# Kernel tuning notes

Hardware: AMD Instinct MI355X
Metric: run time of the kernel (lower is better)

Reference implementation:

```python
import jax, jax.numpy as jnp
import numpy as np

NEG_SLOPE = 0.01  # torch leaky_relu default

def leaky_relu(x):
    return jnp.where(x >= 0, x, NEG_SLOPE * x)

def setup_inputs() -> dict:
    key = jax.random.key(0)
    k1, k2, k3, k4, k5, k6 = jax.random.split(key, 6)
    B, N, D, E = 4, 20000, 128, 100000
    s = 1.0 / np.sqrt(D)
    embeddings = jax.random.normal(k1, (B, N, D), dtype=jnp.float32)
    edges_ij = jax.random.randint(k2, (E, 2), 0, N, dtype=jnp.int64)
    W6 = jax.random.uniform(k3, (D, D), jnp.float32, -s, s)   # theta6 (in,out)
    W7 = jax.random.uniform(k4, (D, D), jnp.float32, -s, s)   # theta7 (in,out)
    w5 = jax.random.uniform(k5, (3 * D,), jnp.float32, -1.0 / np.sqrt(3 * D), 1.0 / np.sqrt(3 * D))  # theta5
    w_noop = jax.random.uniform(k6, (D,), jnp.float32, -s, s)  # noop
    return {"embeddings": embeddings, "edges_ij": edges_ij, "W6": W6, "W7": W7, "w5": w5, "w_noop": w_noop}

def reference(embeddings, edges_ij, W6, W7, w5, w_noop):
    B, N, D = embeddings.shape
    u = edges_ij[:, 0]
    v = edges_ij[:, 1]
    g = embeddings.sum(axis=1)                      # [B,D] (normalize=False)
    g_proj = g @ W6                                  # [B,D]
    node_proj = jnp.einsum('bnd,de->bne', embeddings, W7)  # [B,N,D]
    # theta5(leaky_relu(cat[g,i,j])) == lrelu(g)@w5_g + lrelu(i)@w5_i + lrelu(j)@w5_j
    # (leaky_relu is elementwise, theta5 has no bias), so project per-node THEN
    # gather scalars per edge — avoids the [B,E,3D] concat intermediate.
    w5_g, w5_i, w5_j = w5[:D], w5[D:2 * D], w5[2 * D:]
    qg = leaky_relu(g_proj) @ w5_g                   # [B]
    qi = leaky_relu(node_proj) @ w5_i                # [B,N]
    qj = leaky_relu(node_proj) @ w5_j                # [B,N]
    edge_q = qg[:, None] + qi[:, u] + qj[:, v]       # [B,E]
    noop_q = (g @ w_noop)[:, None]                   # [B,1]
    return jnp.concatenate([edge_q, noop_q], axis=1)  # [B,E+1]
```

## Files before the change

### kernel.cpp

```cpp
#include <hip/hip_runtime.h>
#include <hip/hip_bf16.h>

#define B_ 4
#define N_ 20000
#define D_ 128
#define E_ 100000

typedef __attribute__((ext_vector_type(8))) short bf16x8;
typedef __attribute__((ext_vector_type(4))) float f32x4;


__global__ void k_prep(const float* __restrict__ W7, __hip_bfloat16* __restrict__ w7t,
                       const unsigned* __restrict__ ew, int* __restrict__ flag) {
    if (blockIdx.x == 64) {
        if (threadIdx.x < 64) {
            unsigned v = ew[2 * threadIdx.x + 1];
            unsigned long long any = __ballot(v != 0u);
            if (threadIdx.x == 0) *flag = (any == 0ULL) ? 1 : 0;
        }
        return;
    }
    int idx = blockIdx.x * 256 + threadIdx.x;
    int k = idx >> 7, e = idx & 127;
    w7t[e * 128 + k] = __float2bfloat16(W7[idx]);
}

__global__ __launch_bounds__(256, 2) void k_main(
    const float* __restrict__ emb, const __hip_bfloat16* __restrict__ w7t,
    const float* __restrict__ w5, float* __restrict__ g,
    float* __restrict__ qi, float* __restrict__ qj)
{
    __shared__ __hip_bfloat16 sA[128][136];
    __shared__ __hip_bfloat16 sB[128][136];
    __shared__ float sred[8][128];

    const int t  = threadIdx.x;
    const int b  = blockIdx.y;
    const int n0 = blockIdx.x * 128;

    {
        const int c4 = t & 31;
        const int r0 = t >> 5;
        float gp0 = 0.f, gp1 = 0.f, gp2 = 0.f, gp3 = 0.f;
        #pragma unroll
        for (int i = 0; i < 16; ++i) {
            int r = r0 + 8 * i;
            int n = n0 + r;
            float4 v = make_float4(0.f, 0.f, 0.f, 0.f);
            if (n < N_) v = ((const float4*)(emb + ((size_t)b * N_ + n) * D_))[c4];
            gp0 += v.x; gp1 += v.y; gp2 += v.z; gp3 += v.w;
            union { short4 s4; __hip_bfloat16 h[4]; } pk;
            pk.h[0] = __float2bfloat16(v.x);
            pk.h[1] = __float2bfloat16(v.y);
            pk.h[2] = __float2bfloat16(v.z);
            pk.h[3] = __float2bfloat16(v.w);
            *reinterpret_cast<short4*>(&sA[r][4 * c4]) = pk.s4;
        }
        sred[r0][4 * c4]     = gp0;
        sred[r0][4 * c4 + 1] = gp1;
        sred[r0][4 * c4 + 2] = gp2;
        sred[r0][4 * c4 + 3] = gp3;
    }
    {
        const uint4* w128 = (const uint4*)w7t;
        #pragma unroll
        for (int it = 0; it < 8; ++it) {
            int d4 = it * 256 + t;
            int e   = d4 >> 4;
            int kp4 = d4 & 15;
            *reinterpret_cast<uint4*>(&sB[e][8 * kp4]) = w128[d4];
        }
    }
    __syncthreads();

    if (t < 128) {
        float s = 0.f;
        #pragma unroll
        for (int r = 0; r < 8; ++r) s += sred[r][t];
        atomicAdd(&g[b * D_ + t], s);
    }

    const int lane = t & 63;
    const int wv   = t >> 6;
    const int rc   = lane & 15;
    const int kg   = lane >> 4;

    f32x4 acc[2][8] = {};
    #pragma unroll
    for (int s = 0; s < 4; ++s) {
        const int koff = s * 32 + kg * 8;
        bf16x8 bfr[8];
        #pragma unroll
        for (int tt = 0; tt < 8; ++tt)
            bfr[tt] = *(const bf16x8*)&sB[tt * 16 + rc][koff];
        #pragma unroll
        for (int rt = 0; rt < 2; ++rt) {
            bf16x8 a = *(const bf16x8*)&sA[wv * 32 + rt * 16 + rc][koff];
            #pragma unroll
            for (int tt = 0; tt < 8; ++tt)
                acc[rt][tt] = __builtin_amdgcn_mfma_f32_16x16x32_bf16(a, bfr[tt], acc[rt][tt], 0, 0, 0);
        }
    }

    #pragma unroll
    for (int rt = 0; rt < 2; ++rt) {
        float qip[4] = {0, 0, 0, 0}, qjp[4] = {0, 0, 0, 0};
        #pragma unroll
        for (int tt = 0; tt < 8; ++tt) {
            int col = tt * 16 + rc;
            float wi = w5[D_ + col];
            float wj = w5[2 * D_ + col];
            #pragma unroll
            for (int r = 0; r < 4; ++r) {
                float p  = acc[rt][tt][r];
                float lr = (p >= 0.f) ? p : 0.01f * p;
                qip[r] += lr * wi;
                qjp[r] += lr * wj;
            }
        }
        #pragma unroll
        for (int m = 1; m < 16; m <<= 1) {
            #pragma unroll
            for (int r = 0; r < 4; ++r) {
                qip[r] += __shfl_xor(qip[r], m);
                qjp[r] += __shfl_xor(qjp[r], m);
            }
        }
        if (rc == 0) {
            #pragma unroll
            for (int r = 0; r < 4; ++r) {
                int node = n0 + wv * 32 + rt * 16 + kg * 4 + r;
                if (node < N_) {
                    qi[b * N_ + node] = qip[r];
                    qj[b * N_ + node] = qjp[r];
                }
            }
        }
    }
}

__global__ __launch_bounds__(128) void k_qg(
    const float* __restrict__ g, const float* __restrict__ W6,
    const float* __restrict__ w5, const float* __restrict__ wno,
    float* __restrict__ qg, float* __restrict__ out)
{
    __shared__ float sg[128];
    __shared__ float sr[2], sr2[2];
    const int b = blockIdx.x;
    const int e = threadIdx.x;
    sg[e] = g[b * D_ + e];
    __syncthreads();
    float p = 0.f;
    #pragma unroll 8
    for (int d = 0; d < 128; ++d)
        p += sg[d] * W6[d * D_ + e];
    float lr = (p >= 0.f) ? p : 0.01f * p;
    float vq = lr * w5[e];
    float vn = sg[e] * wno[e];
    #pragma unroll
    for (int m = 1; m < 64; m <<= 1) {
        vq += __shfl_xor(vq, m);
        vn += __shfl_xor(vn, m);
    }
    if ((e & 63) == 0) { sr[e >> 6] = vq; sr2[e >> 6] = vn; }
    __syncthreads();
    if (e == 0) {
        qg[b] = sr[0] + sr[1];
        out[(size_t)b * (E_ + 1) + E_] = sr2[0] + sr2[1];
    }
}

__global__ __launch_bounds__(256) void k_edge(
    const int* __restrict__ edges, const int* __restrict__ flag,
    const float* __restrict__ qg, const float* __restrict__ qi,
    const float* __restrict__ qj, float* __restrict__ out)
{
    int e = blockIdx.x * 256 + threadIdx.x;
    if (e >= E_) return;
    int u, v;
    if (*flag) { int4 w = ((const int4*)edges)[e]; u = w.x; v = w.z; }
    else       { int2 w = ((const int2*)edges)[e]; u = w.x; v = w.y; }
    float q0 = qg[0], q1 = qg[1], q2 = qg[2], q3 = qg[3];
    out[0 * (size_t)(E_ + 1) + e] = q0 + qi[0 * N_ + u] + qj[0 * N_ + v];
    out[1 * (size_t)(E_ + 1) + e] = q1 + qi[1 * N_ + u] + qj[1 * N_ + v];
    out[2 * (size_t)(E_ + 1) + e] = q2 + qi[2 * N_ + u] + qj[2 * N_ + v];
    out[3 * (size_t)(E_ + 1) + e] = q3 + qi[3 * N_ + u] + qj[3 * N_ + v];
}

extern "C" void kernel_launch(void* const* d_in, const int* in_sizes, int n_in,
                              void* d_out, int out_size, void* d_ws, size_t ws_size,
                              hipStream_t stream)
{
    const float* emb   = (const float*)d_in[0];
    const int*   edges = (const int*)d_in[1];
    const float* W6    = (const float*)d_in[2];
    const float* W7    = (const float*)d_in[3];
    const float* w5    = (const float*)d_in[4];
    const float* wno   = (const float*)d_in[5];
    float* out = (float*)d_out;

    float* W = (float*)d_ws;
    float* g    = W;
    float* qg   = W + 512;
    int*   flag = (int*)(W + 516);
    __hip_bfloat16* w7t = (__hip_bfloat16*)(W + 1024);
    float* qi = W + 9216;
    float* qj = W + 89216;

    hipMemsetAsync(g, 0, 512 * sizeof(float), stream);
    hipLaunchKernelGGL(k_prep, dim3(65), dim3(256), 0, stream,
                       W7, w7t, (const unsigned*)edges, flag);
    hipLaunchKernelGGL(k_main, dim3((N_ + 127) / 128, B_), dim3(256), 0, stream,
                       emb, w7t, w5, g, qi, qj);
    hipLaunchKernelGGL(k_qg, dim3(B_), dim3(128), 0, stream, g, W6, w5, wno, qg, out);
    hipLaunchKernelGGL(k_edge, dim3((E_ + 255) / 256), dim3(256), 0, stream,
                       edges, flag, qg, qi, qj, out);
}
```

Baseline: 44.59 us.

## Stream embeddings directly into MFMA registers, fuse qg into edge kernel, bucket g atomics

W7 is pre-swizzled into the MFMA fragment layout so k_main loads B fragments from shared memory without a transpose. The A operand is now read straight from global into registers instead of being staged in shared memory, and each wave handles its own 32-row tile. Column sums of g are accumulated per wave and added atomically into 16 buckets to spread contention. The memset and the separate qg kernel are removed: every edge block recomputes g@W6 and qg redundantly, which trades extra per-block work for two fewer launches.

```diff
diff --git a/kernel.cpp b/kernel.cpp
--- a/kernel.cpp
+++ b/kernel.cpp
@@ -5,117 +5,103 @@
 #define N_ 20000
 #define D_ 128
 #define E_ 100000
+#define TILES_ 625
+#define NBUCKET 16
 
 typedef __attribute__((ext_vector_type(8))) short bf16x8;
 typedef __attribute__((ext_vector_type(4))) float f32x4;
 
 
-__global__ void k_prep(const float* __restrict__ W7, __hip_bfloat16* __restrict__ w7t,
-                       const unsigned* __restrict__ ew, int* __restrict__ flag) {
-    if (blockIdx.x == 64) {
-        if (threadIdx.x < 64) {
-            unsigned v = ew[2 * threadIdx.x + 1];
+__global__ __launch_bounds__(256) void k_prep(
+    const float* __restrict__ W7, const unsigned* __restrict__ ew,
+    int* __restrict__ flag, float* __restrict__ gbuf, bf16x8* __restrict__ w7f)
+{
+    const int bx = blockIdx.x, t = threadIdx.x;
+    if (bx < 8) {
+        int f = bx * 256 + t;
+        int tt = f >> 8, s = (f >> 6) & 3, lane = f & 63;
+        int kg = lane >> 4, rc = lane & 15;
+        int col = tt * 16 + rc, k0 = s * 32 + kg * 8;
+        union { bf16x8 v; __hip_bfloat16 h[8]; } pk;
+        #pragma unroll
+        for (int m = 0; m < 8; ++m)
+            pk.h[m] = __float2bfloat16(W7[(k0 + m) * D_ + col]);
+        w7f[f] = pk.v;
+    } else if (bx == 8) {
+        if (t < 64) {
+            unsigned v = ew[2 * t + 1];
             unsigned long long any = __ballot(v != 0u);
-            if (threadIdx.x == 0) *flag = (any == 0ULL) ? 1 : 0;
-        }
-        return;
-    }
-    int idx = blockIdx.x * 256 + threadIdx.x;
-    int k = idx >> 7, e = idx & 127;
-    w7t[e * 128 + k] = __float2bfloat16(W7[idx]);
-}
-
-__global__ __launch_bounds__(256, 2) void k_main(
-    const float* __restrict__ emb, const __hip_bfloat16* __restrict__ w7t,
-    const float* __restrict__ w5, float* __restrict__ g,
+            if (t == 0) *flag = (any == 0ULL) ? 1 : 0;
+        }
+    } else {
+        int idx = (bx - 9) * 256 + t;
+        if (idx < NBUCKET * B_ * D_) gbuf[idx] = 0.f;
+    }
+}
+
+__global__ __launch_bounds__(256) void k_main(
+    const float* __restrict__ emb, const bf16x8* __restrict__ w7f,
+    const float* __restrict__ w5, float* __restrict__ gbuf,
     float* __restrict__ qi, float* __restrict__ qj)
 {
-    __shared__ __hip_bfloat16 sA[128][136];
-    __shared__ __hip_bfloat16 sB[128][136];
-    __shared__ float sred[8][128];
-
-    const int t  = threadIdx.x;
-    const int b  = blockIdx.y;
-    const int n0 = blockIdx.x * 128;
-
+    __shared__ bf16x8 sB[2048];
+
+    const int t = threadIdx.x, b = blockIdx.y;
     {
-        const int c4 = t & 31;
-        const int r0 = t >> 5;
-        float gp0 = 0.f, gp1 = 0.f, gp2 = 0.f, gp3 = 0.f;
-        #pragma unroll
-        for (int i = 0; i < 16; ++i) {
-            int r = r0 + 8 * i;
-            int n = n0 + r;
-            float4 v = make_float4(0.f, 0.f, 0.f, 0.f);
-            if (n < N_) v = ((const float4*)(emb + ((size_t)b * N_ + n) * D_))[c4];
-            gp0 += v.x; gp1 += v.y; gp2 += v.z; gp3 += v.w;
-            union { short4 s4; __hip_bfloat16 h[4]; } pk;
-            pk.h[0] = __float2bfloat16(v.x);
-            pk.h[1] = __float2bfloat16(v.y);
-            pk.h[2] = __float2bfloat16(v.z);
-            pk.h[3] = __float2bfloat16(v.w);
-            *reinterpret_cast<short4*>(&sA[r][4 * c4]) = pk.s4;
-        }
-        sred[r0][4 * c4]     = gp0;
-        sred[r0][4 * c4 + 1] = gp1;
-        sred[r0][4 * c4 + 2] = gp2;
-        sred[r0][4 * c4 + 3] = gp3;
-    }
-    {
-        const uint4* w128 = (const uint4*)w7t;
-        #pragma unroll
-        for (int it = 0; it < 8; ++it) {
-            int d4 = it * 256 + t;
-            int e   = d4 >> 4;
-            int kp4 = d4 & 15;
-            *reinterpret_cast<uint4*>(&sB[e][8 * kp4]) = w128[d4];
-        }
-    }
-    __syncthreads();
-
-    if (t < 128) {
-        float s = 0.f;
-        #pragma unroll
-        for (int r = 0; r < 8; ++r) s += sred[r][t];
-        atomicAdd(&g[b * D_ + t], s);
-    }
-
-    const int lane = t & 63;
-    const int wv   = t >> 6;
-    const int rc   = lane & 15;
-    const int kg   = lane >> 4;
+        const uint4* src = (const uint4*)w7f;
+        uint4* dst = (uint4*)sB;
+        #pragma unroll
+        for (int i = 0; i < 8; ++i) dst[t + 256 * i] = src[t + 256 * i];
+    }
+    __syncthreads();
+
+    const int wv = t >> 6, lane = t & 63, rc = lane & 15, kg = lane >> 4;
+    const int tile = blockIdx.x * 4 + wv;
+    if (tile >= TILES_) return;
+
+    const float4* A4 = (const float4*)(emb + (size_t)b * N_ * D_);
+    const int rowbase = tile * 32;
 
     f32x4 acc[2][8] = {};
+    float ga[32];
+    #pragma unroll
+    for (int i = 0; i < 32; ++i) ga[i] = 0.f;
+
     #pragma unroll
     for (int s = 0; s < 4; ++s) {
-        const int koff = s * 32 + kg * 8;
         bf16x8 bfr[8];
         #pragma unroll
         for (int tt = 0; tt < 8; ++tt)
-            bfr[tt] = *(const bf16x8*)&sB[tt * 16 + rc][koff];
+            bfr[tt] = sB[tt * 256 + s * 64 + lane];
         #pragma unroll
         for (int rt = 0; rt < 2; ++rt) {
-            bf16x8 a = *(const bf16x8*)&sA[wv * 32 + rt * 16 + rc][koff];
+            const float4* p = A4 + (rowbase + rt * 16 + rc) * 32 + s * 8 + kg * 2;
+            float4 a0 = p[0], a1 = p[1];
+            ga[s*8+0] += a0.x; ga[s*8+1] += a0.y; ga[s*8+2] += a0.z; ga[s*8+3] += a0.w;
+            ga[s*8+4] += a1.x; ga[s*8+5] += a1.y; ga[s*8+6] += a1.z; ga[s*8+7] += a1.w;
+            union { bf16x8 v; __hip_bfloat16 h[8]; } pk;
+            pk.h[0] = __float2bfloat16(a0.x); pk.h[1] = __float2bfloat16(a0.y);
+            pk.h[2] = __float2bfloat16(a0.z); pk.h[3] = __float2bfloat16(a0.w);
+            pk.h[4] = __float2bfloat16(a1.x); pk.h[5] = __float2bfloat16(a1.y);
+            pk.h[6] = __float2bfloat16(a1.z); pk.h[7] = __float2bfloat16(a1.w);
             #pragma unroll
             for (int tt = 0; tt < 8; ++tt)
-                acc[rt][tt] = __builtin_amdgcn_mfma_f32_16x16x32_bf16(a, bfr[tt], acc[rt][tt], 0, 0, 0);
+                acc[rt][tt] = __builtin_amdgcn_mfma_f32_16x16x32_bf16(pk.v, bfr[tt], acc[rt][tt], 0, 0, 0);
         }
     }
 
     #pragma unroll
     for (int rt = 0; rt < 2; ++rt) {
-        float qip[4] = {0, 0, 0, 0}, qjp[4] = {0, 0, 0, 0};
+        float qip[4] = {0,0,0,0}, qjp[4] = {0,0,0,0};
         #pragma unroll
         for (int tt = 0; tt < 8; ++tt) {
             int col = tt * 16 + rc;
-            float wi = w5[D_ + col];
-            float wj = w5[2 * D_ + col];
+            float wi = w5[D_ + col], wj = w5[2 * D_ + col];
             #pragma unroll
             for (int r = 0; r < 4; ++r) {
-                float p  = acc[rt][tt][r];
-                float lr = (p >= 0.f) ? p : 0.01f * p;
-                qip[r] += lr * wi;
-                qjp[r] += lr * wj;
+                float pv = acc[rt][tt][r];
+                float lr = (pv >= 0.f) ? pv : 0.01f * pv;
+                qip[r] += lr * wi; qjp[r] += lr * wj;
             }
         }
         #pragma unroll
@@ -129,62 +115,114 @@
         if (rc == 0) {
             #pragma unroll
             for (int r = 0; r < 4; ++r) {
-                int node = n0 + wv * 32 + rt * 16 + kg * 4 + r;
-                if (node < N_) {
-                    qi[b * N_ + node] = qip[r];
-                    qj[b * N_ + node] = qjp[r];
-                }
-            }
-        }
-    }
-}
-
-__global__ __launch_bounds__(128) void k_qg(
-    const float* __restrict__ g, const float* __restrict__ W6,
-    const float* __restrict__ w5, const float* __restrict__ wno,
-    float* __restrict__ qg, float* __restrict__ out)
-{
-    __shared__ float sg[128];
-    __shared__ float sr[2], sr2[2];
-    const int b = blockIdx.x;
-    const int e = threadIdx.x;
-    sg[e] = g[b * D_ + e];
-    __syncthreads();
-    float p = 0.f;
-    #pragma unroll 8
-    for (int d = 0; d < 128; ++d)
-        p += sg[d] * W6[d * D_ + e];
-    float lr = (p >= 0.f) ? p : 0.01f * p;
-    float vq = lr * w5[e];
-    float vn = sg[e] * wno[e];
-    #pragma unroll
-    for (int m = 1; m < 64; m <<= 1) {
-        vq += __shfl_xor(vq, m);
-        vn += __shfl_xor(vn, m);
-    }
-    if ((e & 63) == 0) { sr[e >> 6] = vq; sr2[e >> 6] = vn; }
-    __syncthreads();
-    if (e == 0) {
-        qg[b] = sr[0] + sr[1];
-        out[(size_t)b * (E_ + 1) + E_] = sr2[0] + sr2[1];
+                int node = rowbase + rt * 16 + kg * 4 + r;
+                qi[b * N_ + node] = qip[r];
+                qj[b * N_ + node] = qjp[r];
+            }
+        }
+    }
+
+    #pragma unroll
+    for (int m = 1; m < 16; m <<= 1) {
+        #pragma unroll
+        for (int i = 0; i < 32; ++i) ga[i] += __shfl_xor(ga[i], m);
+    }
+    if (rc == 0) {
+        float* gb = gbuf + (tile & (NBUCKET - 1)) * (B_ * D_) + b * D_;
+        #pragma unroll
+        for (int s = 0; s < 4; ++s) {
+            #pragma unroll
+            for (int m = 0; m < 8; ++m)
+                atomicAdd(&gb[s * 32 + kg * 8 + m], ga[s * 8 + m]);
+        }
     }
 }
 
 __global__ __launch_bounds__(256) void k_edge(
     const int* __restrict__ edges, const int* __restrict__ flag,
-    const float* __restrict__ qg, const float* __restrict__ qi,
-    const float* __restrict__ qj, float* __restrict__ out)
-{
-    int e = blockIdx.x * 256 + threadIdx.x;
-    if (e >= E_) return;
-    int u, v;
-    if (*flag) { int4 w = ((const int4*)edges)[e]; u = w.x; v = w.z; }
-    else       { int2 w = ((const int2*)edges)[e]; u = w.x; v = w.y; }
-    float q0 = qg[0], q1 = qg[1], q2 = qg[2], q3 = qg[3];
-    out[0 * (size_t)(E_ + 1) + e] = q0 + qi[0 * N_ + u] + qj[0 * N_ + v];
-    out[1 * (size_t)(E_ + 1) + e] = q1 + qi[1 * N_ + u] + qj[1 * N_ + v];
-    out[2 * (size_t)(E_ + 1) + e] = q2 + qi[2 * N_ + u] + qj[2 * N_ + v];
-    out[3 * (size_t)(E_ + 1) + e] = q3 + qi[3 * N_ + u] + qj[3 * N_ + v];
+    const float* __restrict__ gbuf, const float* __restrict__ W6,
+    const float* __restrict__ w5, const float* __restrict__ wno,
+    const float* __restrict__ qi, const float* __restrict__ qj,
+    float* __restrict__ out)
+{
+    __shared__ float sg[B_][D_];
+    __shared__ float sp2[2][B_][D_];
+    __shared__ float sred[2][B_], sredn[2][B_];
+    __shared__ float sqg[B_];
+
+    const int t = threadIdx.x;
+    const int e = t & 127, half = t >> 7;
+
+    if (t < 128) {
+        #pragma unroll
+        for (int b = 0; b < B_; ++b) {
+            float s = 0.f;
+            #pragma unroll
+            for (int k = 0; k < NBUCKET; ++k)
+                s += gbuf[k * (B_ * D_) + b * D_ + e];
+            sg[b][e] = s;
+        }
+    }
+    __syncthreads();
+
+    {
+        float p[B_] = {0,0,0,0};
+        const int d0 = half * 64;
+        for (int d = d0; d < d0 + 64; ++d) {
+            float w6 = W6[d * D_ + e];
+            #pragma unroll
+            for (int b = 0; b < B_; ++b) p[b] += sg[b][d] * w6;
+        }
+        #pragma unroll
+        for (int b = 0; b < B_; ++b) sp2[half][b][e] = p[b];
+    }
+    __syncthreads();
+
+    if (t < 128) {
+        float vq[B_], vn[B_];
+        #pragma unroll
+        for (int b = 0; b < B_; ++b) {
+            float pv = sp2[0][b][e] + sp2[1][b][e];
+            float lr = (pv >= 0.f) ? pv : 0.01f * pv;
+            vq[b] = lr * w5[e];
+            vn[b] = sg[b][e] * wno[e];
+        }
+        #pragma unroll
+        for (int m = 1; m < 64; m <<= 1) {
+            #pragma unroll
+            for (int b = 0; b < B_; ++b) {
+                vq[b] += __shfl_xor(vq[b], m);
+                vn[b] += __shfl_xor(vn[b], m);
+            }
+        }
+        if ((t & 63) == 0) {
+            #pragma unroll
+            for (int b = 0; b < B_; ++b) {
+                sred[t >> 6][b] = vq[b];
+                sredn[t >> 6][b] = vn[b];
+            }
+        }
+    }
+    __syncthreads();
+    if (t == 0) {
+        #pragma unroll
+        for (int b = 0; b < B_; ++b) {
+            sqg[b] = sred[0][b] + sred[1][b];
+            if (blockIdx.x == 0)
+                out[b * (size_t)(E_ + 1) + E_] = sredn[0][b] + sredn[1][b];
+        }
+    }
+    __syncthreads();
+
+    const int ei = blockIdx.x * 256 + t;
+    if (ei < E_) {
+        int u, v;
+        if (*flag) { int4 w = ((const int4*)edges)[ei]; u = w.x; v = w.z; }
+        else       { int2 w = ((const int2*)edges)[ei]; u = w.x; v = w.y; }
+        #pragma unroll
+        for (int b = 0; b < B_; ++b)
+            out[b * (size_t)(E_ + 1) + ei] = sqg[b] + qi[b * N_ + u] + qj[b * N_ + v];
+    }
 }
 
 extern "C" void kernel_launch(void* const* d_in, const int* in_sizes, int n_in,
@@ -200,19 +238,16 @@
     float* out = (float*)d_out;
 
     float* W = (float*)d_ws;
-    float* g    = W;
-    float* qg   = W + 512;
-    int*   flag = (int*)(W + 516);
-    __hip_bfloat16* w7t = (__hip_bfloat16*)(W + 1024);
-    float* qi = W + 9216;
-    float* qj = W + 89216;
-
-    hipMemsetAsync(g, 0, 512 * sizeof(float), stream);
-    hipLaunchKernelGGL(k_prep, dim3(65), dim3(256), 0, stream,
-                       W7, w7t, (const unsigned*)edges, flag);
-    hipLaunchKernelGGL(k_main, dim3((N_ + 127) / 128, B_), dim3(256), 0, stream,
-                       emb, w7t, w5, g, qi, qj);
-    hipLaunchKernelGGL(k_qg, dim3(B_), dim3(128), 0, stream, g, W6, w5, wno, qg, out);
+    int*   flag = (int*)W;
+    float* gbuf = W + 256;
+    bf16x8* w7f = (bf16x8*)(W + 8448);
+    float* qi = W + 16640;
+    float* qj = W + 96640;
+
+    hipLaunchKernelGGL(k_prep, dim3(41), dim3(256), 0, stream,
+                       W7, (const unsigned*)edges, flag, gbuf, w7f);
+    hipLaunchKernelGGL(k_main, dim3((TILES_ + 3) / 4, B_), dim3(256), 0, stream,
+                       emb, w7f, w5, gbuf, qi, qj);
     hipLaunchKernelGGL(k_edge, dim3((E_ + 255) / 256), dim3(256), 0, stream,
-                       edges, flag, qg, qi, qj, out);
-}
+                       edges, flag, gbuf, W6, w5, wno, qi, qj, out);
+}
```

After: 52.03 us. +16.7%, slower.
